# Kernel tuning notes

Hardware: AMD Instinct MI355X
Metric: run time of the kernel (lower is better)

The kernel has to match this reference:

```python
import jax, jax.numpy as jnp
import numpy as np

N, E = 2048, 65536
EMBED, H0, H1 = 64, 128, 128
VOCAB = 625  # 5**k with k=4
SLOPE = 0.01  # F.leaky_relu_ default negative slope


def setup_inputs() -> dict:
    key = jax.random.key(0)
    ks = jax.random.split(key, 20)
    f = jax.random.normal
    return {
        "node_ids": jax.random.randint(ks[0], (N,), 0, VOCAB),
        "edge_index": jax.random.randint(ks[1], (2, E), 0, N),
        "edge_attr": jax.random.uniform(ks[2], (E, 1), dtype=jnp.float32),
        "m": (jax.random.uniform(ks[3], (N, N)) > 0.5).astype(jnp.float32),
        "emb": f(ks[4], (VOCAB, EMBED), dtype=jnp.float32) * 0.1,
        "l0_lin1": f(ks[5], (H0, EMBED + 1), dtype=jnp.float32) * 0.1,
        "l0_lin2": f(ks[6], (H0, H0), dtype=jnp.float32) * 0.1,
        "l0_att_l": f(ks[7], (H0,), dtype=jnp.float32) * 0.1,
        "l0_att_r": f(ks[8], (EMBED,), dtype=jnp.float32) * 0.1,
        "l0_bias": f(ks[9], (H0,), dtype=jnp.float32) * 0.1,
        "l1_lin1": f(ks[10], (H1, H0 + 1), dtype=jnp.float32) * 0.1,
        "l1_lin2": f(ks[11], (H1, H1), dtype=jnp.float32) * 0.1,
        "l1_att_l": f(ks[12], (H1,), dtype=jnp.float32) * 0.1,
        "l1_att_r": f(ks[13], (H0,), dtype=jnp.float32) * 0.1,
        "l1_bias": f(ks[14], (H1,), dtype=jnp.float32) * 0.1,
        "W1": f(ks[15], (20, (EMBED + H0 + H1) * 2), dtype=jnp.float32) * 0.1,
        "b1": f(ks[16], (20,), dtype=jnp.float32) * 0.1,
        "W2": f(ks[17], (20,), dtype=jnp.float32) * 0.1,
        "b2": f(ks[18], (1,), dtype=jnp.float32) * 0.1,
    }


def _segment_softmax(alpha, index, n):
    # numerically-stable softmax over edges grouped by destination node
    amax = jax.ops.segment_max(alpha, index, num_segments=n)
    amax = jnp.where(jnp.isfinite(amax), amax, 0.0)
    e = jnp.exp(alpha - amax[index])
    denom = jax.ops.segment_sum(e, index, num_segments=n)
    return e / (denom[index] + 1e-16)


def _gate_conv(x, src, dst, edge_attr, lin1, lin2, att_l, att_r, bias, n):
    # PyG AttentiveFP GATEConv: message = lin2(leaky_relu(lin1([x_j, e]))) * alpha
    h = jax.nn.leaky_relu(jnp.concatenate([x[src], edge_attr], axis=-1) @ lin1.T, SLOPE)  # [E,out]
    alpha = jax.nn.leaky_relu(h @ att_l + x[dst] @ att_r, SLOPE)  # [E]
    alpha = _segment_softmax(alpha, dst, n)
    msg = (h @ lin2.T) * alpha[:, None]
    return jax.ops.segment_sum(msg, dst, num_segments=n) + bias


def reference(node_ids, edge_index, edge_attr, m, emb,
              l0_lin1, l0_lin2, l0_att_l, l0_att_r, l0_bias,
              l1_lin1, l1_lin2, l1_att_l, l1_att_r, l1_bias,
              W1, b1, W2, b2):
    src, dst = edge_index[0], edge_index[1]
    x = emb[node_ids]  # [N, EMBED]
    h1 = jax.nn.relu(_gate_conv(x, src, dst, edge_attr, l0_lin1, l0_lin2, l0_att_l, l0_att_r, l0_bias, N))
    h2 = jax.nn.relu(_gate_conv(h1, src, dst, edge_attr, l1_lin1, l1_lin2, l1_att_l, l1_att_r, l1_bias, N))
    feat = jnp.concatenate([x, h1, h2], axis=-1)  # [N, C], C = EMBED+H0+H1
    C = feat.shape[-1]
    # 1x1 conv over concat([x_i, x_j]) == split linear: out[c,i,j] = W1[c,:C]@feat[i] + W1[c,C:]@feat[j] + b1[c]
    a = feat @ W1[:, :C].T  # [N, 20] row (i) term
    b = feat @ W1[:, C:].T  # [N, 20] col (j) term
    h = jax.nn.relu(a[:, None, :] + b[None, :, :] + b1)  # [N, N, 20]
    logits = (h @ W2 + b2[0]) * m  # [N, N]; mask multiplies logits as in original
    return jax.nn.softmax(logits, axis=1)
```

## Files before the change

kernel.cpp:

```cpp
#include <hip/hip_runtime.h>
#include <math.h>

#define N 2048
#define E 65536
#define EMBED 64
#define H 128
#define NT 20
#define C3 320
#define CAP 96
#define SLOPE 0.01f

__device__ __forceinline__ float leaky(float x) { return x > 0.f ? x : SLOPE * x; }

__device__ __forceinline__ float wave_sum(float v) {
#pragma unroll
    for (int o = 32; o > 0; o >>= 1) v += __shfl_xor(v, o, 64);
    return v;
}

__global__ __launch_bounds__(256) void k_prep(
    const int* __restrict__ ei, const float* __restrict__ eattr,
    int* __restrict__ cursor, int* __restrict__ srcs, float* __restrict__ eas,
    const float* __restrict__ l1_lin1, float* __restrict__ WT1,
    const float* __restrict__ l0_lin2, float* __restrict__ LT0,
    const float* __restrict__ l1_lin2, float* __restrict__ LT1,
    const int* __restrict__ ids, const float* __restrict__ emb,
    const float* __restrict__ l0_lin1,
    float* __restrict__ x, float* __restrict__ A) {
    int b = blockIdx.x;
    int tid = threadIdx.x;
    if (b < 256) {
        int e = b * 256 + tid;
        int d = ei[E + e];
        int pos = atomicAdd(&cursor[d], 1);
        if (pos < CAP) {
            srcs[d * CAP + pos] = ei[e];
            eas[d * CAP + pos] = eattr[e];
        }
    } else if (b < 448) {
        int j = (b - 256) * 256 + tid;
        if (j < 16384) {
            int c = j >> 7, k = j & 127;
            WT1[j] = l1_lin1[k * (H + 1) + c];
        } else if (j < 32768) {
            int jj = j - 16384; int c = jj >> 7, k = jj & 127;
            LT0[jj] = l0_lin2[k * H + c];
        } else {
            int jj = j - 32768; int c = jj >> 7, k = jj & 127;
            LT1[jj] = l1_lin2[k * H + c];
        }
    } else {
        __shared__ float lw[EMBED][130];
        int n0 = (b - 448) * 8;
        for (int j = tid; j < H * (EMBED + 1); j += 256) {
            int k = j / (EMBED + 1), c = j % (EMBED + 1);
            float v = l0_lin1[j];
            if (c < EMBED) lw[c][k] = v;
        }
        for (int idx = tid; idx < 8 * EMBED; idx += 256) {
            int g = idx >> 6, c = idx & 63;
            x[(n0 + g) * EMBED + c] = emb[ids[n0 + g] * EMBED + c];
        }
        __syncthreads();
        int k = tid & 127, half = tid >> 7;
        const float* xr[4];
#pragma unroll
        for (int it = 0; it < 4; it++) {
            int nn = __builtin_amdgcn_readfirstlane(n0 + 2 * it + half);
            xr[it] = emb + (size_t)ids[nn] * EMBED;
        }
        float acc[4] = {0.f, 0.f, 0.f, 0.f};
#pragma unroll 4
        for (int c = 0; c < EMBED; c++) {
            float wt = lw[c][k];
#pragma unroll
            for (int it = 0; it < 4; it++) acc[it] = fmaf(xr[it][c], wt, acc[it]);
        }
#pragma unroll
        for (int it = 0; it < 4; it++) A[(n0 + 2 * it + half) * H + k] = acc[it];
    }
}

__device__ __forceinline__ void gate_partial(
    int dst, int lane, float xr,
    const float* __restrict__ A,
    float w0, float w1, float attl0, float attl1,
    const int* __restrict__ srcs, const float* __restrict__ eas, int cnt, int i0start,
    float& m_out, float& s_out, float& v0_out, float& v1_out) {
    int c0 = 2 * lane;
    int base = dst * CAP;
    float mmax = -INFINITY, s = 0.f, v0 = 0.f, v1 = 0.f;
    for (int i0 = i0start; i0 < cnt; i0 += 16) {
        int nb = cnt - i0; if (nb > 8) nb = 8;
        float h0[8], h1v[8], p[8];
#pragma unroll
        for (int e = 0; e < 8; e++) {
            float ea = 0.f; float2 av = make_float2(0.f, 0.f);
            if (e < nb) {
                int sn = srcs[base + i0 + e];
                ea = eas[base + i0 + e];
                av = *(const float2*)&A[sn * H + c0];
            }
            h0[e] = leaky(fmaf(w0, ea, av.x));
            h1v[e] = leaky(fmaf(w1, ea, av.y));
            p[e] = h0[e] * attl0 + h1v[e] * attl1;
        }
#pragma unroll
        for (int o = 32; o > 0; o >>= 1) {
#pragma unroll
            for (int e = 0; e < 8; e++) p[e] += __shfl_xor(p[e], o, 64);
        }
        float alpha[8];
#pragma unroll
        for (int e = 0; e < 8; e++)
            alpha[e] = (e < nb) ? leaky(p[e] + xr) : -INFINITY;
        float mb = alpha[0];
#pragma unroll
        for (int e = 1; e < 8; e++) mb = fmaxf(mb, alpha[e]);
        float mnew = fmaxf(mmax, mb);
        float scale = __expf(mmax - mnew);
        float sw = 0.f, sv0 = 0.f, sv1 = 0.f;
#pragma unroll
        for (int e = 0; e < 8; e++) {
            float we = __expf(alpha[e] - mnew);
            sw += we;
            sv0 = fmaf(we, h0[e], sv0);
            sv1 = fmaf(we, h1v[e], sv1);
        }
        s = fmaf(s, scale, sw);
        v0 = fmaf(v0, scale, sv0);
        v1 = fmaf(v1, scale, sv1);
        mmax = mnew;
    }
    m_out = mmax; s_out = s; v0_out = v0; v1_out = v1;
}

__device__ __forceinline__ void gate_merge(
    float mA, float sA, float vA0, float vA1,
    float mB, float sB, float vB0, float vB1,
    float& o0, float& o1) {
    float m = fmaxf(mA, mB);
    if (m == -INFINITY) { o0 = 0.f; o1 = 0.f; return; }
    float eA = __expf(mA - m), eB = __expf(mB - m);
    float inv = 1.f / (fmaf(sA, eA, sB * eB) + 1e-16f);
    o0 = fmaf(vA0, eA, vB0 * eB) * inv;
    o1 = fmaf(vA1, eA, vB1 * eB) * inv;
}

__global__ __launch_bounds__(256, 4) void k_g0(
    const float* __restrict__ x, const float* __restrict__ A0,
    const float* __restrict__ l0_lin1,
    const float* __restrict__ att_l, const float* __restrict__ att_r,
    const int* __restrict__ srcs, const float* __restrict__ eas,
    const int* __restrict__ cursor,
    const float* __restrict__ LT0, const float* __restrict__ b0,
    const float* __restrict__ WT1,
    float* __restrict__ h1, float* __restrict__ A1) {
    __shared__ float vs[4][H];
    __shared__ float pm[4], ps[4];
    __shared__ float agg_s[2][H];
    __shared__ float hs[2][H];
    int n0 = blockIdx.x * 2;
    int tid = threadIdx.x;
    int wv = __builtin_amdgcn_readfirstlane(tid >> 6);
    int lane = tid & 63;
    int c0 = 2 * lane;
    int p = wv >> 1, h = wv & 1;
    int dst = n0 + p;

    float xr = wave_sum(x[dst * EMBED + lane] * att_r[lane]);
    float attl0 = att_l[c0], attl1 = att_l[c0 + 1];
    float w0 = l0_lin1[c0 * (EMBED + 1) + EMBED];
    float w1 = l0_lin1[(c0 + 1) * (EMBED + 1) + EMBED];
    int cnt = cursor[dst]; if (cnt > CAP) cnt = CAP;

    float pm_, ps_, pv0, pv1;
    gate_partial(dst, lane, xr, A0, w0, w1, attl0, attl1, srcs, eas, cnt, h * 8,
                 pm_, ps_, pv0, pv1);
    vs[wv][c0] = pv0; vs[wv][c0 + 1] = pv1;
    if (lane == 0) { pm[wv] = pm_; ps[wv] = ps_; }
    __syncthreads();
    if (h == 0) {
        float o0, o1;
        gate_merge(pm_, ps_, pv0, pv1,
                   pm[wv ^ 1], ps[wv ^ 1], vs[wv ^ 1][c0], vs[wv ^ 1][c0 + 1], o0, o1);
        agg_s[p][c0] = o0;
        agg_s[p][c0 + 1] = o1;
    }
    __syncthreads();

    int k = tid & 127, q = tid >> 7;
    float acc0 = b0[k];
#pragma unroll 2
    for (int ct = 0; ct < H / 4; ct++) {
        float u0 = LT0[(4 * ct + 0) * H + k];
        float u1 = LT0[(4 * ct + 1) * H + k];
        float u2 = LT0[(4 * ct + 2) * H + k];
        float u3 = LT0[(4 * ct + 3) * H + k];
        float4 f0 = *(const float4*)&agg_s[q][4 * ct];
        acc0 = fmaf(f0.x, u0, acc0); acc0 = fmaf(f0.y, u1, acc0);
        acc0 = fmaf(f0.z, u2, acc0); acc0 = fmaf(f0.w, u3, acc0);
    }
    float hv0 = fmaxf(acc0, 0.f);
    h1[(n0 + q) * H + k] = hv0;
    hs[q][k] = hv0;
    __syncthreads();

    float a0 = 0.f;
#pragma unroll 2
    for (int ct = 0; ct < H / 4; ct++) {
        float u0 = WT1[(4 * ct + 0) * H + k];
        float u1 = WT1[(4 * ct + 1) * H + k];
        float u2 = WT1[(4 * ct + 2) * H + k];
        float u3 = WT1[(4 * ct + 3) * H + k];
        float4 f0 = *(const float4*)&hs[q][4 * ct];
        a0 = fmaf(f0.x, u0, a0); a0 = fmaf(f0.y, u1, a0);
        a0 = fmaf(f0.z, u2, a0); a0 = fmaf(f0.w, u3, a0);
    }
    A1[(n0 + q) * H + k] = a0;
}

__global__ __launch_bounds__(256, 4) void k_g1(
    const float* __restrict__ h1g, const float* __restrict__ A1,
    const float* __restrict__ l1_lin1,
    const float* __restrict__ att_l, const float* __restrict__ att_r,
    const int* __restrict__ srcs, const float* __restrict__ eas,
    const int* __restrict__ cursor,
    const float* __restrict__ LT1, const float* __restrict__ bL1,
    const float* __restrict__ x, const float* __restrict__ W1,
    float* __restrict__ aArr, float* __restrict__ bT) {
    __shared__ float vs[4][H];
    __shared__ float pm[4], ps[4];
    __shared__ float agg_s[2][H];
    __shared__ float feat[2][C3];
    int n0 = blockIdx.x * 2;
    int tid = threadIdx.x;
    int wv = __builtin_amdgcn_readfirstlane(tid >> 6);
    int lane = tid & 63;
    int c0 = 2 * lane;
    int p = wv >> 1, h = wv & 1;
    int dst = n0 + p;

    float xr = wave_sum(h1g[dst * H + lane] * att_r[lane] +
                        h1g[dst * H + 64 + lane] * att_r[64 + lane]);
    float attl0 = att_l[c0], attl1 = att_l[c0 + 1];
    float w0 = l1_lin1[c0 * (H + 1) + H];
    float w1 = l1_lin1[(c0 + 1) * (H + 1) + H];
    int cnt = cursor[dst]; if (cnt > CAP) cnt = CAP;

    float pm_, ps_, pv0, pv1;
    gate_partial(dst, lane, xr, A1, w0, w1, attl0, attl1, srcs, eas, cnt, h * 8,
                 pm_, ps_, pv0, pv1);
    vs[wv][c0] = pv0; vs[wv][c0 + 1] = pv1;
    if (lane == 0) { pm[wv] = pm_; ps[wv] = ps_; }
    __syncthreads();
    if (h == 0) {
        float o0, o1;
        gate_merge(pm_, ps_, pv0, pv1,
                   pm[wv ^ 1], ps[wv ^ 1], vs[wv ^ 1][c0], vs[wv ^ 1][c0 + 1], o0, o1);
        agg_s[p][c0] = o0;
        agg_s[p][c0 + 1] = o1;
    }

    for (int idx = tid; idx < 2 * EMBED; idx += 256) {
        int g = idx >> 6, c = idx & 63;
        feat[g][c] = x[(n0 + g) * EMBED + c];
    }
    for (int idx = tid; idx < 2 * H; idx += 256) {
        int g = idx >> 7, c = idx & 127;
        feat[g][EMBED + c] = h1g[(n0 + g) * H + c];
    }
    __syncthreads();

    int k = tid & 127, q = tid >> 7;
    float acc0 = bL1[k];
#pragma unroll 2
    for (int ct = 0; ct < H / 4; ct++) {
        float u0 = LT1[(4 * ct + 0) * H + k];
        float u1 = LT1[(4 * ct + 1) * H + k];
        float u2 = LT1[(4 * ct + 2) * H + k];
        float u3 = LT1[(4 * ct + 3) * H + k];
        float4 f0 = *(const float4*)&agg_s[q][4 * ct];
        acc0 = fmaf(f0.x, u0, acc0); acc0 = fmaf(f0.y, u1, acc0);
        acc0 = fmaf(f0.z, u2, acc0); acc0 = fmaf(f0.w, u3, acc0);
    }
    feat[q][EMBED + H + k] = fmaxf(acc0, 0.f);
    __syncthreads();

    if (tid < 80) {
        int g = tid / 40, u = tid % 40;
        int t = u % 20, side = u / 20;
        const float* wrow = W1 + t * (2 * C3) + side * C3;
        float s = 0.f;
#pragma unroll 4
        for (int ct = 0; ct < C3 / 4; ct++) {
            float4 fv = *(const float4*)&feat[g][4 * ct];
            float4 wv4 = *(const float4*)&wrow[4 * ct];
            s = fmaf(fv.x, wv4.x, s);
            s = fmaf(fv.y, wv4.y, s);
            s = fmaf(fv.z, wv4.z, s);
            s = fmaf(fv.w, wv4.w, s);
        }
        if (side == 0) aArr[(n0 + g) * NT + t] = s;
        else bT[t * N + (n0 + g)] = s;
    }
}

__global__ __launch_bounds__(256, 4) void k_final(const float* __restrict__ aArr,
                                                  const float* __restrict__ bT,
                                                  const float* __restrict__ b1,
                                                  const float* __restrict__ W2,
                                                  const float* __restrict__ b2,
                                                  const float* __restrict__ mmat,
                                                  float* __restrict__ out) {
    __shared__ float red[8];
    int i0 = blockIdx.x * 2;
    int tid = threadIdx.x;
    int lane = tid & 63, wv = tid >> 6;
    float w2r[NT];
#pragma unroll
    for (int t = 0; t < NT; t++) w2r[t] = W2[t];
    float b2v = b2[0];
    float ab[2][NT];
#pragma unroll
    for (int g = 0; g < 2; g++) {
#pragma unroll
        for (int t = 0; t < NT; t++)
            ab[g][t] = aArr[(i0 + g) * NT + t] + b1[t];
    }
    float4 l4[2][2];
    float tmax[2] = {-INFINITY, -INFINITY};
#pragma unroll
    for (int it = 0; it < 2; it++) {
        int j = 4 * tid + 1024 * it;
        float4 s4[2];
#pragma unroll
        for (int g = 0; g < 2; g++) s4[g] = make_float4(b2v, b2v, b2v, b2v);
#pragma unroll
        for (int t = 0; t < NT; t++) {
            float4 bt4 = *(const float4*)&bT[t * N + j];
#pragma unroll
            for (int g = 0; g < 2; g++) {
                float a = ab[g][t], w = w2r[t];
                s4[g].x = fmaf(fmaxf(a + bt4.x, 0.f), w, s4[g].x);
                s4[g].y = fmaf(fmaxf(a + bt4.y, 0.f), w, s4[g].y);
                s4[g].z = fmaf(fmaxf(a + bt4.z, 0.f), w, s4[g].z);
                s4[g].w = fmaf(fmaxf(a + bt4.w, 0.f), w, s4[g].w);
            }
        }
#pragma unroll
        for (int g = 0; g < 2; g++) {
            float4 mm = *(const float4*)&mmat[(size_t)(i0 + g) * N + j];
            s4[g].x *= mm.x; s4[g].y *= mm.y; s4[g].z *= mm.z; s4[g].w *= mm.w;
            l4[g][it] = s4[g];
            tmax[g] = fmaxf(tmax[g], fmaxf(fmaxf(s4[g].x, s4[g].y), fmaxf(s4[g].z, s4[g].w)));
        }
    }
#pragma unroll
    for (int g = 0; g < 2; g++) {
#pragma unroll
        for (int o = 32; o > 0; o >>= 1)
            tmax[g] = fmaxf(tmax[g], __shfl_xor(tmax[g], o, 64));
    }
    if (lane == 0) {
#pragma unroll
        for (int g = 0; g < 2; g++) red[wv * 2 + g] = tmax[g];
    }
    __syncthreads();
    float mfin[2];
#pragma unroll
    for (int g = 0; g < 2; g++)
        mfin[g] = fmaxf(fmaxf(red[g], red[2 + g]), fmaxf(red[4 + g], red[6 + g]));
    __syncthreads();

    float ts[2] = {0.f, 0.f};
#pragma unroll
    for (int it = 0; it < 2; it++) {
#pragma unroll
        for (int g = 0; g < 2; g++) {
            float4 v = l4[g][it];
            v.x = __expf(v.x - mfin[g]);
            v.y = __expf(v.y - mfin[g]);
            v.z = __expf(v.z - mfin[g]);
            v.w = __expf(v.w - mfin[g]);
            l4[g][it] = v;
            ts[g] += v.x + v.y + v.z + v.w;
        }
    }
#pragma unroll
    for (int g = 0; g < 2; g++) {
#pragma unroll
        for (int o = 32; o > 0; o >>= 1) ts[g] += __shfl_xor(ts[g], o, 64);
    }
    if (lane == 0) {
#pragma unroll
        for (int g = 0; g < 2; g++) red[wv * 2 + g] = ts[g];
    }
    __syncthreads();
    float inv[2];
#pragma unroll
    for (int g = 0; g < 2; g++)
        inv[g] = 1.f / (red[g] + red[2 + g] + red[4 + g] + red[6 + g]);

#pragma unroll
    for (int it = 0; it < 2; it++) {
        int j = 4 * tid + 1024 * it;
#pragma unroll
        for (int g = 0; g < 2; g++) {
            float4 v = l4[g][it];
            v.x *= inv[g]; v.y *= inv[g]; v.z *= inv[g]; v.w *= inv[g];
            *(float4*)&out[(size_t)(i0 + g) * N + j] = v;
        }
    }
}

extern "C" void kernel_launch(void* const* d_in, const int* in_sizes, int n_in,
                              void* d_out, int out_size, void* d_ws, size_t ws_size,
                              hipStream_t stream) {
    const int*   node_ids = (const int*)d_in[0];
    const int*   ei       = (const int*)d_in[1];
    const float* eattr    = (const float*)d_in[2];
    const float* mmat     = (const float*)d_in[3];
    const float* emb      = (const float*)d_in[4];
    const float* l0_lin1  = (const float*)d_in[5];
    const float* l0_lin2  = (const float*)d_in[6];
    const float* l0_att_l = (const float*)d_in[7];
    const float* l0_att_r = (const float*)d_in[8];
    const float* l0_bias  = (const float*)d_in[9];
    const float* l1_lin1  = (const float*)d_in[10];
    const float* l1_lin2  = (const float*)d_in[11];
    const float* l1_att_l = (const float*)d_in[12];
    const float* l1_att_r = (const float*)d_in[13];
    const float* l1_bias  = (const float*)d_in[14];
    const float* W1       = (const float*)d_in[15];
    const float* b1       = (const float*)d_in[16];
    const float* W2       = (const float*)d_in[17];
    const float* b2       = (const float*)d_in[18];
    float* out = (float*)d_out;

    char* w = (char*)d_ws;
    auto alloc = [&](size_t bytes) {
        char* p = w;
        w += (bytes + 255) & ~(size_t)255;
        return p;
    };
    int*   cursor = (int*)alloc(N * sizeof(int));
    int*   srcs   = (int*)alloc(N * CAP * sizeof(int));
    float* eas    = (float*)alloc(N * CAP * sizeof(float));
    float* x      = (float*)alloc(N * EMBED * sizeof(float));
    float* A0     = (float*)alloc(N * H * sizeof(float));
    float* A1     = (float*)alloc(N * H * sizeof(float));
    float* h1     = (float*)alloc(N * H * sizeof(float));
    float* aArr   = (float*)alloc(N * NT * sizeof(float));
    float* bT     = (float*)alloc(NT * N * sizeof(float));
    float* WT1    = (float*)alloc(H * H * sizeof(float));
    float* LT0    = (float*)alloc(H * H * sizeof(float));
    float* LT1    = (float*)alloc(H * H * sizeof(float));

    hipMemsetAsync(cursor, 0, N * sizeof(int), stream);

    k_prep<<<704, 256, 0, stream>>>(ei, eattr, cursor, srcs, eas,
                                    l1_lin1, WT1, l0_lin2, LT0, l1_lin2, LT1,
                                    node_ids, emb, l0_lin1, x, A0);
    k_g0<<<N / 2, 256, 0, stream>>>(x, A0, l0_lin1, l0_att_l, l0_att_r,
                                    srcs, eas, cursor, LT0, l0_bias, WT1, h1, A1);
    k_g1<<<N / 2, 256, 0, stream>>>(h1, A1, l1_lin1, l1_att_l, l1_att_r,
                                    srcs, eas, cursor, LT1, l1_bias, x, W1, aArr, bT);
    k_final<<<N / 2, 256, 0, stream>>>(aArr, bT, b1, W2, b2, mmat, out);
}
```

Baseline: 187.0 us.

## Fuse four kernels into one persistent kernel with software grid barriers

Replaces the prep, two gate-conv, and final softmax kernels with a single 1024-block kernel that separates its phases with atomic-counter grid barriers. The goal is to remove launch overhead and inter-kernel gaps. The A0 projection is now computed per block from global memory instead of through a shared-memory transposed weight tile. This relies on all 1024 blocks being co-resident, which is not guaranteed without a cooperative launch, so it risks deadlock and adds spin-wait cost.

New measurement: 488.2 us. 2.61x slower.

```diff
diff --git a/kernel.cpp b/kernel.cpp
--- a/kernel.cpp
+++ b/kernel.cpp
@@ -9,6 +9,8 @@
 #define C3 320
 #define CAP 96
 #define SLOPE 0.01f
+#define NBLK 1024
+#define NTHR 256
 
 __device__ __forceinline__ float leaky(float x) { return x > 0.f ? x : SLOPE * x; }
 
@@ -18,67 +20,16 @@
     return v;
 }
 
-__global__ __launch_bounds__(256) void k_prep(
-    const int* __restrict__ ei, const float* __restrict__ eattr,
-    int* __restrict__ cursor, int* __restrict__ srcs, float* __restrict__ eas,
-    const float* __restrict__ l1_lin1, float* __restrict__ WT1,
-    const float* __restrict__ l0_lin2, float* __restrict__ LT0,
-    const float* __restrict__ l1_lin2, float* __restrict__ LT1,
-    const int* __restrict__ ids, const float* __restrict__ emb,
-    const float* __restrict__ l0_lin1,
-    float* __restrict__ x, float* __restrict__ A) {
-    int b = blockIdx.x;
-    int tid = threadIdx.x;
-    if (b < 256) {
-        int e = b * 256 + tid;
-        int d = ei[E + e];
-        int pos = atomicAdd(&cursor[d], 1);
-        if (pos < CAP) {
-            srcs[d * CAP + pos] = ei[e];
-            eas[d * CAP + pos] = eattr[e];
-        }
-    } else if (b < 448) {
-        int j = (b - 256) * 256 + tid;
-        if (j < 16384) {
-            int c = j >> 7, k = j & 127;
-            WT1[j] = l1_lin1[k * (H + 1) + c];
-        } else if (j < 32768) {
-            int jj = j - 16384; int c = jj >> 7, k = jj & 127;
-            LT0[jj] = l0_lin2[k * H + c];
-        } else {
-            int jj = j - 32768; int c = jj >> 7, k = jj & 127;
-            LT1[jj] = l1_lin2[k * H + c];
-        }
-    } else {
-        __shared__ float lw[EMBED][130];
-        int n0 = (b - 448) * 8;
-        for (int j = tid; j < H * (EMBED + 1); j += 256) {
-            int k = j / (EMBED + 1), c = j % (EMBED + 1);
-            float v = l0_lin1[j];
-            if (c < EMBED) lw[c][k] = v;
-        }
-        for (int idx = tid; idx < 8 * EMBED; idx += 256) {
-            int g = idx >> 6, c = idx & 63;
-            x[(n0 + g) * EMBED + c] = emb[ids[n0 + g] * EMBED + c];
-        }
-        __syncthreads();
-        int k = tid & 127, half = tid >> 7;
-        const float* xr[4];
-#pragma unroll
-        for (int it = 0; it < 4; it++) {
-            int nn = __builtin_amdgcn_readfirstlane(n0 + 2 * it + half);
-            xr[it] = emb + (size_t)ids[nn] * EMBED;
-        }
-        float acc[4] = {0.f, 0.f, 0.f, 0.f};
-#pragma unroll 4
-        for (int c = 0; c < EMBED; c++) {
-            float wt = lw[c][k];
-#pragma unroll
-            for (int it = 0; it < 4; it++) acc[it] = fmaf(xr[it][c], wt, acc[it]);
-        }
-#pragma unroll
-        for (int it = 0; it < 4; it++) A[(n0 + 2 * it + half) * H + k] = acc[it];
-    }
+__device__ __forceinline__ void grid_sync(int* bar, int target) {
+    __syncthreads();
+    if (threadIdx.x == 0) {
+        __builtin_amdgcn_fence(__ATOMIC_RELEASE, "agent");
+        __hip_atomic_fetch_add(bar, 1, __ATOMIC_RELAXED, __HIP_MEMORY_SCOPE_AGENT);
+        while (__hip_atomic_load(bar, __ATOMIC_RELAXED, __HIP_MEMORY_SCOPE_AGENT) < target)
+            __builtin_amdgcn_s_sleep(2);
+        __builtin_amdgcn_fence(__ATOMIC_ACQUIRE, "agent");
+    }
+    __syncthreads();
 }
 
 __device__ __forceinline__ void gate_partial(
@@ -147,269 +98,302 @@
     o1 = fmaf(vA1, eA, vB1 * eB) * inv;
 }
 
-__global__ __launch_bounds__(256, 4) void k_g0(
-    const float* __restrict__ x, const float* __restrict__ A0,
-    const float* __restrict__ l0_lin1,
-    const float* __restrict__ att_l, const float* __restrict__ att_r,
-    const int* __restrict__ srcs, const float* __restrict__ eas,
-    const int* __restrict__ cursor,
-    const float* __restrict__ LT0, const float* __restrict__ b0,
-    const float* __restrict__ WT1,
-    float* __restrict__ h1, float* __restrict__ A1) {
+__global__ __launch_bounds__(NTHR) void k_fused(
+    const int* __restrict__ ids, const int* __restrict__ ei,
+    const float* __restrict__ eattr, const float* __restrict__ mmat,
+    const float* __restrict__ emb,
+    const float* __restrict__ l0_lin1, const float* __restrict__ l0_lin2,
+    const float* __restrict__ l0_att_l, const float* __restrict__ l0_att_r,
+    const float* __restrict__ l0_bias,
+    const float* __restrict__ l1_lin1, const float* __restrict__ l1_lin2,
+    const float* __restrict__ l1_att_l, const float* __restrict__ l1_att_r,
+    const float* __restrict__ l1_bias,
+    const float* __restrict__ W1, const float* __restrict__ b1,
+    const float* __restrict__ W2, const float* __restrict__ b2,
+    int* __restrict__ cursor, int* __restrict__ bar,
+    int* __restrict__ srcs, float* __restrict__ eas,
+    float* __restrict__ x, float* __restrict__ A0, float* __restrict__ A1,
+    float* __restrict__ h1, float* __restrict__ aArr, float* __restrict__ bT,
+    float* __restrict__ WT1, float* __restrict__ LT0, float* __restrict__ LT1,
+    float* __restrict__ out) {
     __shared__ float vs[4][H];
     __shared__ float pm[4], ps[4];
     __shared__ float agg_s[2][H];
-    __shared__ float hs[2][H];
-    int n0 = blockIdx.x * 2;
-    int tid = threadIdx.x;
-    int wv = __builtin_amdgcn_readfirstlane(tid >> 6);
-    int lane = tid & 63;
-    int c0 = 2 * lane;
-    int p = wv >> 1, h = wv & 1;
-    int dst = n0 + p;
-
-    float xr = wave_sum(x[dst * EMBED + lane] * att_r[lane]);
-    float attl0 = att_l[c0], attl1 = att_l[c0 + 1];
-    float w0 = l0_lin1[c0 * (EMBED + 1) + EMBED];
-    float w1 = l0_lin1[(c0 + 1) * (EMBED + 1) + EMBED];
-    int cnt = cursor[dst]; if (cnt > CAP) cnt = CAP;
-
-    float pm_, ps_, pv0, pv1;
-    gate_partial(dst, lane, xr, A0, w0, w1, attl0, attl1, srcs, eas, cnt, h * 8,
-                 pm_, ps_, pv0, pv1);
-    vs[wv][c0] = pv0; vs[wv][c0 + 1] = pv1;
-    if (lane == 0) { pm[wv] = pm_; ps[wv] = ps_; }
-    __syncthreads();
-    if (h == 0) {
-        float o0, o1;
-        gate_merge(pm_, ps_, pv0, pv1,
-                   pm[wv ^ 1], ps[wv ^ 1], vs[wv ^ 1][c0], vs[wv ^ 1][c0 + 1], o0, o1);
-        agg_s[p][c0] = o0;
-        agg_s[p][c0 + 1] = o1;
-    }
-    __syncthreads();
-
-    int k = tid & 127, q = tid >> 7;
-    float acc0 = b0[k];
+    __shared__ float big[2][C3];
+    __shared__ float red[8];
+    const int b = blockIdx.x;
+    const int tid = threadIdx.x;
+    const int gtid = b * NTHR + tid;
+
+    if (gtid < E) {
+        int d = ei[E + gtid];
+        int pos = atomicAdd(&cursor[d], 1);
+        if (pos < CAP) {
+            srcs[d * CAP + pos] = ei[gtid];
+            eas[d * CAP + pos] = eattr[gtid];
+        }
+    }
+    if (gtid < 16384) {
+        WT1[gtid] = l1_lin1[(gtid & 127) * (H + 1) + (gtid >> 7)];
+    } else if (gtid < 32768) {
+        int j = gtid - 16384;
+        LT0[j] = l0_lin2[(j & 127) * H + (j >> 7)];
+    } else if (gtid < 49152) {
+        int j = gtid - 32768;
+        LT1[j] = l1_lin2[(j & 127) * H + (j >> 7)];
+    }
+    if (gtid < N * EMBED) {
+        int g = gtid >> 6, c = gtid & 63;
+        x[gtid] = emb[ids[g] * EMBED + c];
+    }
+    {
+        int n0 = b * 2;
+        int k = tid & 127, q = tid >> 7;
+        int nn = __builtin_amdgcn_readfirstlane(n0 + q);
+        const float* xr = emb + (size_t)ids[nn] * EMBED;
+        const float* wr = l0_lin1 + k * (EMBED + 1);
+        float acc = 0.f;
+#pragma unroll 4
+        for (int c = 0; c < EMBED; c++)
+            acc = fmaf(xr[c], wr[c], acc);
+        A0[(n0 + q) * H + k] = acc;
+    }
+    grid_sync(bar, NBLK);
+
+    {
+        float (*hs)[H] = (float(*)[H])big;
+        int n0 = b * 2;
+        int wv = __builtin_amdgcn_readfirstlane(tid >> 6);
+        int lane = tid & 63;
+        int c0 = 2 * lane;
+        int p = wv >> 1, h = wv & 1;
+        int dst = n0 + p;
+
+        float xr = wave_sum(x[dst * EMBED + lane] * l0_att_r[lane]);
+        float attl0 = l0_att_l[c0], attl1 = l0_att_l[c0 + 1];
+        float w0 = l0_lin1[c0 * (EMBED + 1) + EMBED];
+        float w1 = l0_lin1[(c0 + 1) * (EMBED + 1) + EMBED];
+        int cnt = cursor[dst]; if (cnt > CAP) cnt = CAP;
+
+        float pm_, ps_, pv0, pv1;
+        gate_partial(dst, lane, xr, A0, w0, w1, attl0, attl1, srcs, eas, cnt, h * 8,
+                     pm_, ps_, pv0, pv1);
+        vs[wv][c0] = pv0; vs[wv][c0 + 1] = pv1;
+        if (lane == 0) { pm[wv] = pm_; ps[wv] = ps_; }
+        __syncthreads();
+        if (h == 0) {
+            float o0, o1;
+            gate_merge(pm_, ps_, pv0, pv1,
+                       pm[wv ^ 1], ps[wv ^ 1], vs[wv ^ 1][c0], vs[wv ^ 1][c0 + 1], o0, o1);
+            agg_s[p][c0] = o0;
+            agg_s[p][c0 + 1] = o1;
+        }
+        __syncthreads();
+
+        int k = tid & 127, q = tid >> 7;
+        float acc0 = l0_bias[k];
 #pragma unroll 2
-    for (int ct = 0; ct < H / 4; ct++) {
-        float u0 = LT0[(4 * ct + 0) * H + k];
-        float u1 = LT0[(4 * ct + 1) * H + k];
-        float u2 = LT0[(4 * ct + 2) * H + k];
-        float u3 = LT0[(4 * ct + 3) * H + k];
-        float4 f0 = *(const float4*)&agg_s[q][4 * ct];
-        acc0 = fmaf(f0.x, u0, acc0); acc0 = fmaf(f0.y, u1, acc0);
-        acc0 = fmaf(f0.z, u2, acc0); acc0 = fmaf(f0.w, u3, acc0);
-    }
-    float hv0 = fmaxf(acc0, 0.f);
-    h1[(n0 + q) * H + k] = hv0;
-    hs[q][k] = hv0;
-    __syncthreads();
-
-    float a0 = 0.f;
+        for (int ct = 0; ct < H / 4; ct++) {
+            float u0 = LT0[(4 * ct + 0) * H + k];
+            float u1 = LT0[(4 * ct + 1) * H + k];
+            float u2 = LT0[(4 * ct + 2) * H + k];
+            float u3 = LT0[(4 * ct + 3) * H + k];
+            float4 f0 = *(const float4*)&agg_s[q][4 * ct];
+            acc0 = fmaf(f0.x, u0, acc0); acc0 = fmaf(f0.y, u1, acc0);
+            acc0 = fmaf(f0.z, u2, acc0); acc0 = fmaf(f0.w, u3, acc0);
+        }
+        float hv0 = fmaxf(acc0, 0.f);
+        h1[(n0 + q) * H + k] = hv0;
+        hs[q][k] = hv0;
+        __syncthreads();
+
+        float a0 = 0.f;
 #pragma unroll 2
-    for (int ct = 0; ct < H / 4; ct++) {
-        float u0 = WT1[(4 * ct + 0) * H + k];
-        float u1 = WT1[(4 * ct + 1) * H + k];
-        float u2 = WT1[(4 * ct + 2) * H + k];
-        float u3 = WT1[(4 * ct + 3) * H + k];
-        float4 f0 = *(const float4*)&hs[q][4 * ct];
-        a0 = fmaf(f0.x, u0, a0); a0 = fmaf(f0.y, u1, a0);
-        a0 = fmaf(f0.z, u2, a0); a0 = fmaf(f0.w, u3, a0);
-    }
-    A1[(n0 + q) * H + k] = a0;
-}
-
-__global__ __launch_bounds__(256, 4) void k_g1(
-    const float* __restrict__ h1g, const float* __restrict__ A1,
-    const float* __restrict__ l1_lin1,
-    const float* __restrict__ att_l, const float* __restrict__ att_r,
-    const int* __restrict__ srcs, const float* __restrict__ eas,
-    const int* __restrict__ cursor,
-    const float* __restrict__ LT1, const float* __restrict__ bL1,
-    const float* __restrict__ x, const float* __restrict__ W1,
-    float* __restrict__ aArr, float* __restrict__ bT) {
-    __shared__ float vs[4][H];
-    __shared__ float pm[4], ps[4];
-    __shared__ float agg_s[2][H];
-    __shared__ float feat[2][C3];
-    int n0 = blockIdx.x * 2;
-    int tid = threadIdx.x;
-    int wv = __builtin_amdgcn_readfirstlane(tid >> 6);
-    int lane = tid & 63;
-    int c0 = 2 * lane;
-    int p = wv >> 1, h = wv & 1;
-    int dst = n0 + p;
-
-    float xr = wave_sum(h1g[dst * H + lane] * att_r[lane] +
-                        h1g[dst * H + 64 + lane] * att_r[64 + lane]);
-    float attl0 = att_l[c0], attl1 = att_l[c0 + 1];
-    float w0 = l1_lin1[c0 * (H + 1) + H];
-    float w1 = l1_lin1[(c0 + 1) * (H + 1) + H];
-    int cnt = cursor[dst]; if (cnt > CAP) cnt = CAP;
-
-    float pm_, ps_, pv0, pv1;
-    gate_partial(dst, lane, xr, A1, w0, w1, attl0, attl1, srcs, eas, cnt, h * 8,
-                 pm_, ps_, pv0, pv1);
-    vs[wv][c0] = pv0; vs[wv][c0 + 1] = pv1;
-    if (lane == 0) { pm[wv] = pm_; ps[wv] = ps_; }
-    __syncthreads();
-    if (h == 0) {
-        float o0, o1;
-        gate_merge(pm_, ps_, pv0, pv1,
-                   pm[wv ^ 1], ps[wv ^ 1], vs[wv ^ 1][c0], vs[wv ^ 1][c0 + 1], o0, o1);
-        agg_s[p][c0] = o0;
-        agg_s[p][c0 + 1] = o1;
-    }
-
-    for (int idx = tid; idx < 2 * EMBED; idx += 256) {
-        int g = idx >> 6, c = idx & 63;
-        feat[g][c] = x[(n0 + g) * EMBED + c];
-    }
-    for (int idx = tid; idx < 2 * H; idx += 256) {
-        int g = idx >> 7, c = idx & 127;
-        feat[g][EMBED + c] = h1g[(n0 + g) * H + c];
-    }
-    __syncthreads();
-
-    int k = tid & 127, q = tid >> 7;
-    float acc0 = bL1[k];
+        for (int ct = 0; ct < H / 4; ct++) {
+            float u0 = WT1[(4 * ct + 0) * H + k];
+            float u1 = WT1[(4 * ct + 1) * H + k];
+            float u2 = WT1[(4 * ct + 2) * H + k];
+            float u3 = WT1[(4 * ct + 3) * H + k];
+            float4 f0 = *(const float4*)&hs[q][4 * ct];
+            a0 = fmaf(f0.x, u0, a0); a0 = fmaf(f0.y, u1, a0);
+            a0 = fmaf(f0.z, u2, a0); a0 = fmaf(f0.w, u3, a0);
+        }
+        A1[(n0 + q) * H + k] = a0;
+    }
+    grid_sync(bar, 2 * NBLK);
+
+    {
+        float (*feat)[C3] = big;
+        int n0 = b * 2;
+        int wv = __builtin_amdgcn_readfirstlane(tid >> 6);
+        int lane = tid & 63;
+        int c0 = 2 * lane;
+        int p = wv >> 1, h = wv & 1;
+        int dst = n0 + p;
+
+        float xr = wave_sum(h1[dst * H + lane] * l1_att_r[lane] +
+                            h1[dst * H + 64 + lane] * l1_att_r[64 + lane]);
+        float attl0 = l1_att_l[c0], attl1 = l1_att_l[c0 + 1];
+        float w0 = l1_lin1[c0 * (H + 1) + H];
+        float w1 = l1_lin1[(c0 + 1) * (H + 1) + H];
+        int cnt = cursor[dst]; if (cnt > CAP) cnt = CAP;
+
+        float pm_, ps_, pv0, pv1;
+        gate_partial(dst, lane, xr, A1, w0, w1, attl0, attl1, srcs, eas, cnt, h * 8,
+                     pm_, ps_, pv0, pv1);
+        vs[wv][c0] = pv0; vs[wv][c0 + 1] = pv1;
+        if (lane == 0) { pm[wv] = pm_; ps[wv] = ps_; }
+        __syncthreads();
+        if (h == 0) {
+            float o0, o1;
+            gate_merge(pm_, ps_, pv0, pv1,
+                       pm[wv ^ 1], ps[wv ^ 1], vs[wv ^ 1][c0], vs[wv ^ 1][c0 + 1], o0, o1);
+            agg_s[p][c0] = o0;
+            agg_s[p][c0 + 1] = o1;
+        }
+
+        for (int idx = tid; idx < 2 * EMBED; idx += NTHR) {
+            int g = idx >> 6, c = idx & 63;
+            feat[g][c] = x[(n0 + g) * EMBED + c];
+        }
+        for (int idx = tid; idx < 2 * H; idx += NTHR) {
+            int g = idx >> 7, c = idx & 127;
+            feat[g][EMBED + c] = h1[(n0 + g) * H + c];
+        }
+        __syncthreads();
+
+        int k = tid & 127, q = tid >> 7;
+        float acc0 = l1_bias[k];
 #pragma unroll 2
-    for (int ct = 0; ct < H / 4; ct++) {
-        float u0 = LT1[(4 * ct + 0) * H + k];
-        float u1 = LT1[(4 * ct + 1) * H + k];
-        float u2 = LT1[(4 * ct + 2) * H + k];
-        float u3 = LT1[(4 * ct + 3) * H + k];
-        float4 f0 = *(const float4*)&agg_s[q][4 * ct];
-        acc0 = fmaf(f0.x, u0, acc0); acc0 = fmaf(f0.y, u1, acc0);
-        acc0 = fmaf(f0.z, u2, acc0); acc0 = fmaf(f0.w, u3, acc0);
-    }
-    feat[q][EMBED + H + k] = fmaxf(acc0, 0.f);
-    __syncthreads();
-
-    if (tid < 80) {
-        int g = tid / 40, u = tid % 40;
-        int t = u % 20, side = u / 20;
-        const float* wrow = W1 + t * (2 * C3) + side * C3;
-        float s = 0.f;
+        for (int ct = 0; ct < H / 4; ct++) {
+            float u0 = LT1[(4 * ct + 0) * H + k];
+            float u1 = LT1[(4 * ct + 1) * H + k];
+            float u2 = LT1[(4 * ct + 2) * H + k];
+            float u3 = LT1[(4 * ct + 3) * H + k];
+            float4 f0 = *(const float4*)&agg_s[q][4 * ct];
+            acc0 = fmaf(f0.x, u0, acc0); acc0 = fmaf(f0.y, u1, acc0);
+            acc0 = fmaf(f0.z, u2, acc0); acc0 = fmaf(f0.w, u3, acc0);
+        }
+        feat[q][EMBED + H + k] = fmaxf(acc0, 0.f);
+        __syncthreads();
+
+        if (tid < 80) {
+            int g = tid / 40, u = tid % 40;
+            int t = u % 20, side = u / 20;
+            const float* wrow = W1 + t * (2 * C3) + side * C3;
+            float s = 0.f;
 #pragma unroll 4
-        for (int ct = 0; ct < C3 / 4; ct++) {
-            float4 fv = *(const float4*)&feat[g][4 * ct];
-            float4 wv4 = *(const float4*)&wrow[4 * ct];
-            s = fmaf(fv.x, wv4.x, s);
-            s = fmaf(fv.y, wv4.y, s);
-            s = fmaf(fv.z, wv4.z, s);
-            s = fmaf(fv.w, wv4.w, s);
-        }
-        if (side == 0) aArr[(n0 + g) * NT + t] = s;
-        else bT[t * N + (n0 + g)] = s;
-    }
-}
-
-__global__ __launch_bounds__(256, 4) void k_final(const float* __restrict__ aArr,
-                                                  const float* __restrict__ bT,
-                                                  const float* __restrict__ b1,
-                                                  const float* __restrict__ W2,
-                                                  const float* __restrict__ b2,
-                                                  const float* __restrict__ mmat,
-                                                  float* __restrict__ out) {
-    __shared__ float red[8];
-    int i0 = blockIdx.x * 2;
-    int tid = threadIdx.x;
-    int lane = tid & 63, wv = tid >> 6;
-    float w2r[NT];
-#pragma unroll
-    for (int t = 0; t < NT; t++) w2r[t] = W2[t];
-    float b2v = b2[0];
-    float ab[2][NT];
-#pragma unroll
-    for (int g = 0; g < 2; g++) {
-#pragma unroll
-        for (int t = 0; t < NT; t++)
-            ab[g][t] = aArr[(i0 + g) * NT + t] + b1[t];
-    }
-    float4 l4[2][2];
-    float tmax[2] = {-INFINITY, -INFINITY};
-#pragma unroll
-    for (int it = 0; it < 2; it++) {
-        int j = 4 * tid + 1024 * it;
-        float4 s4[2];
-#pragma unroll
-        for (int g = 0; g < 2; g++) s4[g] = make_float4(b2v, b2v, b2v, b2v);
-#pragma unroll
-        for (int t = 0; t < NT; t++) {
-            float4 bt4 = *(const float4*)&bT[t * N + j];
+            for (int ct = 0; ct < C3 / 4; ct++) {
+                float4 fv = *(const float4*)&feat[g][4 * ct];
+                float4 wv4 = *(const float4*)&wrow[4 * ct];
+                s = fmaf(fv.x, wv4.x, s);
+                s = fmaf(fv.y, wv4.y, s);
+                s = fmaf(fv.z, wv4.z, s);
+                s = fmaf(fv.w, wv4.w, s);
+            }
+            if (side == 0) aArr[(n0 + g) * NT + t] = s;
+            else bT[t * N + (n0 + g)] = s;
+        }
+    }
+    grid_sync(bar, 3 * NBLK);
+
+    {
+        int i0 = b * 2;
+        int lane = tid & 63, wv = tid >> 6;
+        float w2r[NT];
+#pragma unroll
+        for (int t = 0; t < NT; t++) w2r[t] = W2[t];
+        float b2v = b2[0];
+        float ab[2][NT];
+#pragma unroll
+        for (int g = 0; g < 2; g++) {
+#pragma unroll
+            for (int t = 0; t < NT; t++)
+                ab[g][t] = aArr[(i0 + g) * NT + t] + b1[t];
+        }
+        float4 l4[2][2];
+        float tmax[2] = {-INFINITY, -INFINITY};
+#pragma unroll
+        for (int it = 0; it < 2; it++) {
+            int j = 4 * tid + 1024 * it;
+            float4 s4[2];
+#pragma unroll
+            for (int g = 0; g < 2; g++) s4[g] = make_float4(b2v, b2v, b2v, b2v);
+#pragma unroll
+            for (int t = 0; t < NT; t++) {
+                float4 bt4 = *(const float4*)&bT[t * N + j];
+#pragma unroll
+                for (int g = 0; g < 2; g++) {
+                    float a = ab[g][t], w = w2r[t];
+                    s4[g].x = fmaf(fmaxf(a + bt4.x, 0.f), w, s4[g].x);
+                    s4[g].y = fmaf(fmaxf(a + bt4.y, 0.f), w, s4[g].y);
+                    s4[g].z = fmaf(fmaxf(a + bt4.z, 0.f), w, s4[g].z);
+                    s4[g].w = fmaf(fmaxf(a + bt4.w, 0.f), w, s4[g].w);
+                }
+            }
 #pragma unroll
             for (int g = 0; g < 2; g++) {
-                float a = ab[g][t], w = w2r[t];
-                s4[g].x = fmaf(fmaxf(a + bt4.x, 0.f), w, s4[g].x);
-                s4[g].y = fmaf(fmaxf(a + bt4.y, 0.f), w, s4[g].y);
-                s4[g].z = fmaf(fmaxf(a + bt4.z, 0.f), w, s4[g].z);
-                s4[g].w = fmaf(fmaxf(a + bt4.w, 0.f), w, s4[g].w);
+                float4 mm = *(const float4*)&mmat[(size_t)(i0 + g) * N + j];
+                s4[g].x *= mm.x; s4[g].y *= mm.y; s4[g].z *= mm.z; s4[g].w *= mm.w;
+                l4[g][it] = s4[g];
+                tmax[g] = fmaxf(tmax[g], fmaxf(fmaxf(s4[g].x, s4[g].y), fmaxf(s4[g].z, s4[g].w)));
             }
         }
 #pragma unroll
         for (int g = 0; g < 2; g++) {
-            float4 mm = *(const float4*)&mmat[(size_t)(i0 + g) * N + j];
-            s4[g].x *= mm.x; s4[g].y *= mm.y; s4[g].z *= mm.z; s4[g].w *= mm.w;
-            l4[g][it] = s4[g];
-            tmax[g] = fmaxf(tmax[g], fmaxf(fmaxf(s4[g].x, s4[g].y), fmaxf(s4[g].z, s4[g].w)));
-        }
-    }
-#pragma unroll
-    for (int g = 0; g < 2; g++) {
-#pragma unroll
-        for (int o = 32; o > 0; o >>= 1)
-            tmax[g] = fmaxf(tmax[g], __shfl_xor(tmax[g], o, 64));
-    }
-    if (lane == 0) {
-#pragma unroll
-        for (int g = 0; g < 2; g++) red[wv * 2 + g] = tmax[g];
-    }
-    __syncthreads();
-    float mfin[2];
-#pragma unroll
-    for (int g = 0; g < 2; g++)
-        mfin[g] = fmaxf(fmaxf(red[g], red[2 + g]), fmaxf(red[4 + g], red[6 + g]));
-    __syncthreads();
-
-    float ts[2] = {0.f, 0.f};
-#pragma unroll
-    for (int it = 0; it < 2; it++) {
+#pragma unroll
+            for (int o = 32; o > 0; o >>= 1)
+                tmax[g] = fmaxf(tmax[g], __shfl_xor(tmax[g], o, 64));
+        }
+        if (lane == 0) {
+#pragma unroll
+            for (int g = 0; g < 2; g++) red[wv * 2 + g] = tmax[g];
+        }
+        __syncthreads();
+        float mfin[2];
+#pragma unroll
+        for (int g = 0; g < 2; g++)
+            mfin[g] = fmaxf(fmaxf(red[g], red[2 + g]), fmaxf(red[4 + g], red[6 + g]));
+        __syncthreads();
+
+        float ts[2] = {0.f, 0.f};
+#pragma unroll
+        for (int it = 0; it < 2; it++) {
+#pragma unroll
+            for (int g = 0; g < 2; g++) {
+                float4 v = l4[g][it];
+                v.x = __expf(v.x - mfin[g]);
+                v.y = __expf(v.y - mfin[g]);
+                v.z = __expf(v.z - mfin[g]);
+                v.w = __expf(v.w - mfin[g]);
+                l4[g][it] = v;
+                ts[g] += v.x + v.y + v.z + v.w;
+            }
+        }
 #pragma unroll
         for (int g = 0; g < 2; g++) {
-            float4 v = l4[g][it];
-            v.x = __expf(v.x - mfin[g]);
-            v.y = __expf(v.y - mfin[g]);
-            v.z = __expf(v.z - mfin[g]);
-            v.w = __expf(v.w - mfin[g]);
-            l4[g][it] = v;
-            ts[g] += v.x + v.y + v.z + v.w;
-        }
-    }
-#pragma unroll
-    for (int g = 0; g < 2; g++) {
-#pragma unroll
-        for (int o = 32; o > 0; o >>= 1) ts[g] += __shfl_xor(ts[g], o, 64);
-    }
-    if (lane == 0) {
-#pragma unroll
-        for (int g = 0; g < 2; g++) red[wv * 2 + g] = ts[g];
-    }
-    __syncthreads();
-    float inv[2];
-#pragma unroll
-    for (int g = 0; g < 2; g++)
-        inv[g] = 1.f / (red[g] + red[2 + g] + red[4 + g] + red[6 + g]);
-
-#pragma unroll
-    for (int it = 0; it < 2; it++) {
-        int j = 4 * tid + 1024 * it;
-#pragma unroll
-        for (int g = 0; g < 2; g++) {
-            float4 v = l4[g][it];
-            v.x *= inv[g]; v.y *= inv[g]; v.z *= inv[g]; v.w *= inv[g];
-            *(float4*)&out[(size_t)(i0 + g) * N + j] = v;
+#pragma unroll
+            for (int o = 32; o > 0; o >>= 1) ts[g] += __shfl_xor(ts[g], o, 64);
+        }
+        if (lane == 0) {
+#pragma unroll
+            for (int g = 0; g < 2; g++) red[wv * 2 + g] = ts[g];
+        }
+        __syncthreads();
+        float inv[2];
+#pragma unroll
+        for (int g = 0; g < 2; g++)
+            inv[g] = 1.f / (red[g] + red[2 + g] + red[4 + g] + red[6 + g]);
+
+#pragma unroll
+        for (int it = 0; it < 2; it++) {
+            int j = 4 * tid + 1024 * it;
+#pragma unroll
+            for (int g = 0; g < 2; g++) {
+                float4 v = l4[g][it];
+                v.x *= inv[g]; v.y *= inv[g]; v.z *= inv[g]; v.w *= inv[g];
+                *(float4*)&out[(size_t)(i0 + g) * N + j] = v;
+            }
         }
     }
 }
@@ -444,7 +428,8 @@
         w += (bytes + 255) & ~(size_t)255;
         return p;
     };
-    int*   cursor = (int*)alloc(N * sizeof(int));
+    int*   cursor = (int*)alloc((N + 64) * sizeof(int));
+    int*   bar    = cursor + N;
     int*   srcs   = (int*)alloc(N * CAP * sizeof(int));
     float* eas    = (float*)alloc(N * CAP * sizeof(float));
     float* x      = (float*)alloc(N * EMBED * sizeof(float));
@@ -457,14 +442,12 @@
     float* LT0    = (float*)alloc(H * H * sizeof(float));
     float* LT1    = (float*)alloc(H * H * sizeof(float));
 
-    hipMemsetAsync(cursor, 0, N * sizeof(int), stream);
-
-    k_prep<<<704, 256, 0, stream>>>(ei, eattr, cursor, srcs, eas,
-                                    l1_lin1, WT1, l0_lin2, LT0, l1_lin2, LT1,
-                                    node_ids, emb, l0_lin1, x, A0);
-    k_g0<<<N / 2, 256, 0, stream>>>(x, A0, l0_lin1, l0_att_l, l0_att_r,
-                                    srcs, eas, cursor, LT0, l0_bias, WT1, h1, A1);
-    k_g1<<<N / 2, 256, 0, stream>>>(h1, A1, l1_lin1, l1_att_l, l1_att_r,
-                                    srcs, eas, cursor, LT1, l1_bias, x, W1, aArr, bT);
-    k_final<<<N / 2, 256, 0, stream>>>(aArr, bT, b1, W2, b2, mmat, out);
-}
+    hipMemsetAsync(cursor, 0, (N + 64) * sizeof(int), stream);
+
+    k_fused<<<NBLK, NTHR, 0, stream>>>(node_ids, ei, eattr, mmat, emb,
+                                       l0_lin1, l0_lin2, l0_att_l, l0_att_r, l0_bias,
+                                       l1_lin1, l1_lin2, l1_att_l, l1_att_r, l1_bias,
+                                       W1, b1, W2, b2,
+                                       cursor, bar, srcs, eas, x, A0, A1, h1,
+                                       aArr, bT, WT1, LT0, LT1, out);
+}
```
